# Kernel optimization log

Hardware: AMD Instinct MI355X
Metric: run time of the kernel (lower is better)

Reference implementation:

```python
import jax, jax.numpy as jnp
import numpy as np

NOISE_EPS = 1e-2   # Shazeer noisy-gating stddev floor
LN_EPS = 1e-6
LOSS_COEF = 0.01
K = 2              # num_activated_experts


def _layer_norm(x, w, b):
    mu = jnp.mean(x, axis=-1, keepdims=True)
    var = jnp.var(x, axis=-1, keepdims=True)
    return (x - mu) * jax.lax.rsqrt(var + LN_EPS) * w + b


def _cv_squared(v):
    return jnp.var(v) / (jnp.mean(v) ** 2 + 1e-10)


def _normal_cdf(z):
    return 0.5 * (1.0 + jax.scipy.special.erf(z / jnp.sqrt(jnp.asarray(2.0, z.dtype))))


def setup_inputs() -> dict:
    key = jax.random.key(0)
    ks = jax.random.split(key, 8)
    N, D, H, O, E = 8192, 512, 1024, 512, 8
    x = jax.random.normal(ks[0], (N, D), jnp.float32)
    x_offsets = jnp.sort(jax.random.randint(ks[1], (17,), 0, N)).astype(jnp.int64)
    noise = jax.random.normal(ks[2], (N, E), jnp.float32)
    s = 0.02
    return {
        "x": x,
        "x_offsets": x_offsets,
        "max_seq_len": 2048,
        "noise": noise,
        "norm_w": jnp.ones((D,), jnp.float32),
        "norm_bias": jnp.zeros((D,), jnp.float32),
        "w_gate": jax.random.normal(ks[3], (D, E), jnp.float32) * s,
        "w_noise": jax.random.normal(ks[4], (D, E), jnp.float32) * s,
        "W1": jax.random.normal(ks[5], (E, H, D), jnp.float32) * s,  # [E, model_d, input]
        "b1": jnp.zeros((E, H), jnp.float32),
        "W2": jax.random.normal(ks[6], (E, O, H), jnp.float32) * s,  # [E, output, model_d]
        "b2": jnp.zeros((E, O), jnp.float32),
        "output_weight": jax.random.normal(ks[7], (D, O), jnp.float32) * s,
    }


def reference(x, x_offsets, max_seq_len, noise, norm_w, norm_bias, w_gate, w_noise,
              W1, b1, W2, b2, output_weight):
    N, D = x.shape
    E = w_gate.shape[1]
    k_plus = min(K + 1, E)

    # pre-norm
    x_norm = _layer_norm(x, norm_w, norm_bias)

    # noisy top-k gating (training path)
    clean_logits = x_norm @ w_gate                      # [N, E]
    noise_stddev = jax.nn.softplus(x_norm @ w_noise) + NOISE_EPS
    noisy_logits = clean_logits + noise * noise_stddev

    top_logits, top_indices = jax.lax.top_k(noisy_logits, k_plus)   # [N, k+1]
    top_k_logits = top_logits[:, :K]
    top_k_indices = top_indices[:, :K]
    top_k_gates = jax.nn.softmax(top_k_logits, axis=-1)             # [N, K]

    rows = jnp.arange(N)[:, None]
    gates = jnp.zeros((N, E), top_k_gates.dtype).at[rows, top_k_indices].set(top_k_gates)

    # load = prob each expert is in top-k under the gating noise (Shazeer)
    flat = top_logits.reshape(-1)
    pos_in = jnp.arange(N) * k_plus + K
    thr_in = flat[pos_in][:, None]          # (k+1)-th value: threshold if already in
    thr_out = flat[pos_in - 1][:, None]     # k-th value: threshold if currently out
    is_in = noisy_logits > thr_in
    prob_in = _normal_cdf((clean_logits - thr_in) / noise_stddev)
    prob_out = _normal_cdf((clean_logits - thr_out) / noise_stddev)
    load_probs = jnp.where(is_in, prob_in, prob_out)                # [N, E]

    loss = LOSS_COEF * (_cv_squared(gates.sum(0)) + _cv_squared(load_probs.sum(0)))

    # dispatch stats: tokens per expert
    lengths = jnp.zeros((E,), jnp.float32).at[top_k_indices.reshape(-1)].add(1.0)
    load = lengths / lengths.sum()

    # grouped expert MLP (dense one-hot combine; gates are 0 for unrouted experts)
    h = jnp.einsum('nd,ehd->neh', x_norm, W1) + b1                  # [N, E, H]
    a = jax.nn.silu(h)
    y_e = jnp.einsum('neh,eoh->neo', a, W2) + b2                    # [N, E, O]
    y_moe = jnp.einsum('ne,neo->no', gates, y_e)                    # [N, O]

    # shared expert: addmm(y, shared_x=x, output_weight)
    y = y_moe + x @ output_weight
    return y, loss, load
```

## Files before the change

### kernel.cpp

```cpp
#include <hip/hip_runtime.h>
#include <math.h>

typedef unsigned short u16;
typedef unsigned int u32;

#define N_ROWS 8192
#define DDIM 512
#define HDIM 1024
#define ODIM 512
#define NEXP 8
#define MAXPAIRS (N_ROWS * 2)
#define MAXPOS (MAXPAIRS + NEXP * 128)
#define MAXTILES (MAXPOS / 128)

#define SM_CNT 0
#define SM_CUR 8
#define SM_AOFF 16
#define SM_WORDS 64

using short8 = __attribute__((ext_vector_type(8))) short;
using float4v = __attribute__((ext_vector_type(4))) float;

__device__ __forceinline__ u16 f2bf(float f) {
    union { float f; u32 u; } v; v.f = f;
    u32 u = v.u;
    return (u16)((u + 0x7fffu + ((u >> 16) & 1u)) >> 16);
}

__device__ __forceinline__ void async_copy16(u16* lds, const u16* g) {
    __builtin_amdgcn_global_load_lds(
        (const __attribute__((address_space(1))) void*)g,
        (__attribute__((address_space(3))) void*)lds, 16, 0, 0);
}

#define MEGA_GATE 512
#define MEGA_W1 2048
#define MEGA_OWT 256
#define MEGA_BUCKET 68
#define MEGA_W2 2048
#define MEGA_BLOCKS (MEGA_GATE + MEGA_W1 + MEGA_OWT + MEGA_BUCKET + MEGA_W2)
__global__ __launch_bounds__(256) void mega_kernel(
    const float* __restrict__ x, const float* __restrict__ noise,
    const float* __restrict__ norm_w, const float* __restrict__ norm_b,
    const float* __restrict__ w_gate, const float* __restrict__ w_noise,
    const float* __restrict__ W1, const float* __restrict__ ow,
    const float* __restrict__ W2,
    u16* __restrict__ xnorm_bf, u16* __restrict__ x_bf,
    int* __restrict__ pair_expert, float* __restrict__ pair_gate,
    u16* __restrict__ W1b, u16* __restrict__ owT, u16* __restrict__ W2b,
    int* __restrict__ bucket_rows, int* __restrict__ small, float* __restrict__ zeropage,
    float* __restrict__ partial_g, float* __restrict__ partial_l, int* __restrict__ partial_c)
{
    __shared__ __align__(16) float sh[32 * 33 + 8];
    int b = blockIdx.x, tid = threadIdx.x;

    if (b >= MEGA_GATE) {
        int cb = b - MEGA_GATE;
        if (cb < MEGA_W1) {
            size_t i = (size_t)cb * 512 + tid;
#pragma unroll
            for (int t = 0; t < 2; t++, i += 256) {
                float4 v = ((const float4*)W1)[i];
                ushort4 o;
                o.x = f2bf(v.x); o.y = f2bf(v.y); o.z = f2bf(v.z); o.w = f2bf(v.w);
                ((ushort4*)W1b)[i] = o;
            }
        } else if (cb < MEGA_W1 + MEGA_OWT) {
            float (*tile)[33] = (float(*)[33])sh;
            int t = cb - MEGA_W1;
            int bx = (t & 15) * 32, by = (t >> 4) * 32;
            int tx = tid & 31, ty = tid >> 5;
            for (int r = ty; r < 32; r += 8) tile[r][tx] = ow[(size_t)(by + r) * ODIM + bx + tx];
            __syncthreads();
            for (int r = ty; r < 32; r += 8) owT[(size_t)(bx + r) * DDIM + by + tx] = f2bf(tile[tx][r]);
        } else if (cb < MEGA_W1 + MEGA_OWT + MEGA_BUCKET) {
            int lb = cb - MEGA_W1 - MEGA_OWT;
            int i = lb * 256 + tid;
            if (i < MAXPOS) bucket_rows[i] = -1;
            if (lb == 0) {
                if (tid < SM_WORDS) small[tid] = 0;
                zeropage[tid] = 0.f; zeropage[tid + 256] = 0.f;
            }
        } else {
            int j = cb - MEGA_W1 - MEGA_OWT - MEGA_BUCKET;
            size_t i = (size_t)j * 512 + tid;
#pragma unroll
            for (int t = 0; t < 2; t++, i += 256) {
                float4 v = ((const float4*)W2)[i];
                ushort4 o;
                o.x = f2bf(v.x); o.y = f2bf(v.y); o.z = f2bf(v.z); o.w = f2bf(v.w);
                ((ushort4*)W2b)[i] = o;
            }
        }
        return;
    }

    float* lg = sh;
    float* blk_g = sh + 16 * 17;
    float* blk_l = blk_g + 8;
    int* blk_c = (int*)(blk_l + 8);

    int wave = tid >> 6, lane = tid & 63;
    if (tid < 8) { blk_g[tid] = 0.f; blk_l[tid] = 0.f; blk_c[tid] = 0; }
    float nw[8], nb[8];
#pragma unroll
    for (int j = 0; j < 8; j++) { nw[j] = norm_w[j * 64 + lane]; nb[j] = norm_b[j * 64 + lane]; }

    bool l5 = (lane & 32) != 0, l4 = (lane & 16) != 0;
    bool l3 = (lane & 8) != 0, l2 = (lane & 4) != 0;

    for (int half = 0; half < 2; ++half) {
        float xv[2][8], mu[2], rstd[2];
#pragma unroll
        for (int r = 0; r < 2; ++r) {
            int row = b * 16 + wave * 4 + half * 2 + r;
            const float* xr = x + (size_t)row * DDIM;
            float s = 0.f, s2 = 0.f;
#pragma unroll
            for (int j = 0; j < 8; j++) { float v = xr[j * 64 + lane]; xv[r][j] = v; s += v; s2 += v * v; }
#pragma unroll
            for (int o = 32; o; o >>= 1) { s += __shfl_xor(s, o, 64); s2 += __shfl_xor(s2, o, 64); }
            mu[r] = s * (1.f / DDIM);
            float var = s2 * (1.f / DDIM) - mu[r] * mu[r];
            rstd[r] = rsqrtf(var + 1e-6f);
        }
        float acc[2][16];
#pragma unroll
        for (int r = 0; r < 2; ++r)
#pragma unroll
            for (int e = 0; e < 16; e++) acc[r][e] = 0.f;
#pragma unroll
        for (int j = 0; j < 8; j++) {
            int d = j * 64 + lane;
            float4 wg0 = *(const float4*)&w_gate[d * 8];
            float4 wg1 = *(const float4*)&w_gate[d * 8 + 4];
            float4 wn0 = *(const float4*)&w_noise[d * 8];
            float4 wn1 = *(const float4*)&w_noise[d * 8 + 4];
#pragma unroll
            for (int r = 0; r < 2; ++r) {
                int row = b * 16 + wave * 4 + half * 2 + r;
                float v = (xv[r][j] - mu[r]) * rstd[r] * nw[j] + nb[j];
                xnorm_bf[(size_t)row * DDIM + d] = f2bf(v);
                x_bf[(size_t)row * DDIM + d] = f2bf(xv[r][j]);
                acc[r][0] += v * wg0.x; acc[r][1] += v * wg0.y;
                acc[r][2] += v * wg0.z; acc[r][3] += v * wg0.w;
                acc[r][4] += v * wg1.x; acc[r][5] += v * wg1.y;
                acc[r][6] += v * wg1.z; acc[r][7] += v * wg1.w;
                acc[r][8] += v * wn0.x; acc[r][9] += v * wn0.y;
                acc[r][10] += v * wn0.z; acc[r][11] += v * wn0.w;
                acc[r][12] += v * wn1.x; acc[r][13] += v * wn1.y;
                acc[r][14] += v * wn1.z; acc[r][15] += v * wn1.w;
            }
        }
#pragma unroll
        for (int r = 0; r < 2; ++r) {
            int lrow16 = wave * 4 + half * 2 + r;
            float t8[8];
#pragma unroll
            for (int v = 0; v < 8; v++) {
                float snd = l5 ? acc[r][v] : acc[r][v + 8];
                float kp = l5 ? acc[r][v + 8] : acc[r][v];
                t8[v] = kp + __shfl_xor(snd, 32, 64);
            }
            float t4[4];
#pragma unroll
            for (int v = 0; v < 4; v++) {
                float snd = l4 ? t8[v] : t8[v + 4];
                float kp = l4 ? t8[v + 4] : t8[v];
                t4[v] = kp + __shfl_xor(snd, 16, 64);
            }
            float t2[2];
#pragma unroll
            for (int v = 0; v < 2; v++) {
                float snd = l3 ? t4[v] : t4[v + 2];
                float kp = l3 ? t4[v + 2] : t4[v];
                t2[v] = kp + __shfl_xor(snd, 8, 64);
            }
            float snd = l2 ? t2[0] : t2[1];
            float kp = l2 ? t2[1] : t2[0];
            float t1 = kp + __shfl_xor(snd, 4, 64);
            t1 += __shfl_xor(t1, 2, 64);
            t1 += __shfl_xor(t1, 1, 64);
            if ((lane & 3) == 0) lg[lrow16 * 17 + ((lane >> 2) & 15)] = t1;
        }
    }
    __syncthreads();

    if (tid < 16) {
        int row = b * 16 + tid;
        float cl[8], sd[8], nz[8];
#pragma unroll
        for (int e = 0; e < 8; e++) {
            cl[e] = lg[tid * 17 + e];
            float t = lg[tid * 17 + 8 + e];
            float sp = fmaxf(t, 0.f) + log1pf(expf(-fabsf(t)));
            sd[e] = sp + 0.01f;
            nz[e] = cl[e] + noise[(size_t)row * NEXP + e] * sd[e];
        }
        int idx[3]; float val[3]; u32 msk = 0;
#pragma unroll
        for (int t = 0; t < 3; t++) {
            float best = -INFINITY; int bi = 0;
#pragma unroll
            for (int e = 0; e < 8; e++)
                if (!((msk >> e) & 1) && nz[e] > best) { best = nz[e]; bi = e; }
            idx[t] = bi; val[t] = best; msk |= 1u << bi;
        }
        float e1 = expf(val[1] - val[0]);
        float g0 = 1.f / (1.f + e1), g1 = e1 / (1.f + e1);
        float thr_in = val[2], thr_out = val[1];

        pair_expert[row * 2] = idx[0]; pair_gate[row * 2] = g0;
        pair_expert[row * 2 + 1] = idx[1]; pair_gate[row * 2 + 1] = g1;
        atomicAdd(&blk_g[idx[0]], g0); atomicAdd(&blk_g[idx[1]], g1);
        atomicAdd(&blk_c[idx[0]], 1); atomicAdd(&blk_c[idx[1]], 1);
#pragma unroll
        for (int e = 0; e < 8; e++) {
            float thr = (nz[e] > thr_in) ? thr_in : thr_out;
            float z = (cl[e] - thr) / sd[e];
            float p = 0.5f * (1.f + erff(z * 0.70710678118654752f));
            atomicAdd(&blk_l[e], p);
        }
    }
    __syncthreads();
    if (tid < 8) {
        partial_g[b * 8 + tid] = blk_g[tid];
        partial_l[b * 8 + tid] = blk_l[tid];
        partial_c[b * 8 + tid] = blk_c[tid];
    }
}

__global__ __launch_bounds__(256) void scatter_kernel(
    const int* __restrict__ pair_expert, const float* __restrict__ pair_gate,
    const float* __restrict__ partial_g, const float* __restrict__ partial_l,
    const int* __restrict__ partial_c,
    int* __restrict__ small, int* __restrict__ bucket_rows, float* __restrict__ gate_by_pos,
    int* __restrict__ rowpos,
    float* __restrict__ out_loss, float* __restrict__ out_load)
{
    __shared__ int aoff[NEXP + 1];
    __shared__ int blk_cnt[NEXP];
    __shared__ int blk_base[NEXP];
    __shared__ int ired[256];
    __shared__ float fred[256];
    __shared__ float gsum[NEXP], lsum[NEXP];
    int tid = threadIdx.x;
    int e = tid & 7, g = tid >> 3;

    int s = 0;
    for (int k = g; k < MEGA_GATE; k += 32) s += partial_c[k * 8 + e];
    ired[tid] = s;
    if (tid < NEXP) blk_cnt[tid] = 0;
    __syncthreads();
    if (tid < 64) ired[tid] = ired[tid] + ired[tid + 64] + ired[tid + 128] + ired[tid + 192];
    __syncthreads();
    if (tid < 8) {
        int t = 0;
        for (int q = tid; q < 64; q += 8) t += ired[q];
        ired[tid] = t;
    }
    __syncthreads();
    if (tid == 0) {
        int acc = 0; aoff[0] = 0;
        for (int k = 0; k < NEXP; k++) { acc += (ired[k] + 127) & ~127; aoff[k + 1] = acc; }
    }
    __syncthreads();

    int p = blockIdx.x * 256 + tid;
    int pe = pair_expert[p];
    int local = atomicAdd(&blk_cnt[pe], 1);
    __syncthreads();
    if (tid < NEXP)
        blk_base[tid] = aoff[tid] + atomicAdd(&small[SM_CUR + tid], blk_cnt[tid]);
    if (blockIdx.x == 0 && tid < NEXP + 1) small[SM_AOFF + tid] = aoff[tid];
    __syncthreads();
    int pos = blk_base[pe] + local;
    bucket_rows[pos] = p >> 1;
    gate_by_pos[pos] = pair_gate[p];
    rowpos[p] = pos;

    if (blockIdx.x == 0) {
        float sg = 0.f, sl = 0.f;
        for (int k = g; k < MEGA_GATE; k += 32) { sg += partial_g[k * 8 + e]; sl += partial_l[k * 8 + e]; }
        fred[tid] = sg;
        __syncthreads();
        if (tid < 64) fred[tid] = fred[tid] + fred[tid + 64] + fred[tid + 128] + fred[tid + 192];
        __syncthreads();
        if (tid < 8) { float t = 0.f; for (int q = tid; q < 64; q += 8) t += fred[q]; gsum[tid] = t; }
        __syncthreads();
        fred[tid] = sl;
        __syncthreads();
        if (tid < 64) fred[tid] = fred[tid] + fred[tid + 64] + fred[tid + 128] + fred[tid + 192];
        __syncthreads();
        if (tid < 8) { float t = 0.f; for (int q = tid; q < 64; q += 8) t += fred[q]; lsum[tid] = t; }
        __syncthreads();
        if (tid == 0) {
            float cv[2];
            for (int t = 0; t < 2; t++) {
                const float* v = t ? lsum : gsum;
                float m = 0.f;
                for (int k = 0; k < NEXP; k++) m += v[k];
                m *= (1.f / NEXP);
                float var = 0.f;
                for (int k = 0; k < NEXP; k++) { float d = v[k] - m; var += d * d; }
                var *= (1.f / NEXP);
                cv[t] = var / (m * m + 1e-10f);
            }
            out_loss[0] = 0.01f * (cv[0] + cv[1]);
            int tot = 0;
            for (int k = 0; k < NEXP; k++) tot += ired[k];
            float inv = 1.f / (float)tot;
            for (int k = 0; k < NEXP; k++) out_load[k] = (float)ired[k] * inv;
        }
    }
}

__global__ __launch_bounds__(256) void gemmA_kernel(
    const u16* __restrict__ xnorm, const u16* __restrict__ W1b,
    const u16* __restrict__ xbf, const u16* __restrict__ owT,
    const int* __restrict__ bucket_rows, const int* __restrict__ small,
    const float* __restrict__ b1, const u16* __restrict__ zeropage,
    u16* __restrict__ a_buf, float* __restrict__ y)
{
    constexpr int KD = 512;
    __shared__ __align__(16) u16 As[128 * 64];
    __shared__ __align__(16) u16 Bs[128 * 64];

    int tid = threadIdx.x;
    if (blockIdx.y >= 8) {
        int j = (blockIdx.y - 8) * 136 + blockIdx.x;
        if (j >= 256) return;
        int base = (j >> 2) * 128, bn = (j & 3) * 128;
        int wave = tid >> 6, lane = tid & 63;
        const int lrow = lane >> 2;
        const int kcol = (((lane & 3) ^ ((lane >> 3) & 3)) * 8);
        const int trow = wave * 32 + lrow;
        int wm = (wave & 1) * 64, wn = (wave >> 1) * 64;
        int fr = lane & 15, kq = lane >> 4;
        const int kg = ((kq ^ ((fr >> 1) & 3)) * 8);
        const u16* ga0 = xbf + (size_t)(base + trow) * KD + kcol;
        const u16* ga1 = xbf + (size_t)(base + trow + 16) * KD + kcol;
        const u16* gb0 = owT + (size_t)(bn + trow) * KD + kcol;
        const u16* gb1 = owT + (size_t)(bn + trow + 16) * KD + kcol;
        u16* As2 = (u16*)As; u16* Bs2 = (u16*)Bs;
        const int ofA0 = (wave * 32) * 32, ofA1 = (wave * 32 + 16) * 32;

        float4v acc[4][4];
#pragma unroll
        for (int i = 0; i < 4; i++)
#pragma unroll
            for (int jj = 0; jj < 4; jj++) acc[i][jj] = (float4v){0.f, 0.f, 0.f, 0.f};

        async_copy16(As2 + ofA0, ga0); async_copy16(As2 + ofA1, ga1);
        async_copy16(Bs2 + ofA0, gb0); async_copy16(Bs2 + ofA1, gb1);
        __syncthreads();
        int cur = 0;
        for (int t = 0; t < 16; ++t) {
            int nxt = cur ^ 1;
            if (t + 1 < 16) {
                int k1 = (t + 1) << 5;
                async_copy16(As2 + nxt * 4096 + ofA0, ga0 + k1);
                async_copy16(As2 + nxt * 4096 + ofA1, ga1 + k1);
                async_copy16(Bs2 + nxt * 4096 + ofA0, gb0 + k1);
                async_copy16(Bs2 + nxt * 4096 + ofA1, gb1 + k1);
            }
            short8 af[4], bf[4];
#pragma unroll
            for (int mt = 0; mt < 4; mt++) af[mt] = *(const short8*)&As2[cur * 4096 + (wm + mt * 16 + fr) * 32 + kg];
#pragma unroll
            for (int nt = 0; nt < 4; nt++) bf[nt] = *(const short8*)&Bs2[cur * 4096 + (wn + nt * 16 + fr) * 32 + kg];
#pragma unroll
            for (int mt = 0; mt < 4; mt++)
#pragma unroll
                for (int nt = 0; nt < 4; nt++)
                    acc[mt][nt] = __builtin_amdgcn_mfma_f32_16x16x32_bf16(af[mt], bf[nt], acc[mt][nt], 0, 0, 0);
            __syncthreads();
            cur = nxt;
        }
        int rbase = (lane >> 4) * 4, c16 = lane & 15;
#pragma unroll
        for (int mt = 0; mt < 4; mt++) {
            int gm = base + wm + mt * 16 + rbase;
#pragma unroll
            for (int nt = 0; nt < 4; nt++) {
                int gn = bn + wn + nt * 16 + c16;
#pragma unroll
                for (int r = 0; r < 4; r++)
                    y[(size_t)(gm + r) * ODIM + gn] = acc[mt][nt][r];
            }
        }
        return;
    }

    int base = blockIdx.x * 128;
    if (base >= small[SM_AOFF + 8]) return;
    int e = 0;
    while (e < 7 && base >= small[SM_AOFF + e + 1]) ++e;
    int bn = blockIdx.y * 128;
    const u16* Bsel = W1b + (size_t)e * HDIM * KD;

    int wave = tid >> 6, lane = tid & 63;
    int lr = lane >> 3;
    int lc = ((lane & 7) ^ lr) * 8;

    const u16* ga[4]; const u16* gb[4];
    u16* la[4]; u16* lb[4];
#pragma unroll
    for (int c = 0; c < 4; c++) {
        int tr = wave * 32 + c * 8;
        int r0 = bucket_rows[base + tr + lr];
        ga[c] = ((r0 < 0) ? zeropage : xnorm + (size_t)r0 * KD) + lc;
        gb[c] = Bsel + (size_t)(bn + tr + lr) * KD + lc;
        la[c] = &As[tr * 64];
        lb[c] = &Bs[tr * 64];
    }

    int wm = (wave & 1) * 64, wn = (wave >> 1) * 64;
    int fr = lane & 15, kq = lane >> 4, f7 = fr & 7;

    float4v acc[4][4];
#pragma unroll
    for (int i = 0; i < 4; i++)
#pragma unroll
        for (int j = 0; j < 4; j++) acc[i][j] = (float4v){0.f, 0.f, 0.f, 0.f};

    for (int k0 = 0; k0 < KD; k0 += 64) {
        __syncthreads();
#pragma unroll
        for (int c = 0; c < 4; c++) async_copy16(la[c], ga[c] + k0);
#pragma unroll
        for (int c = 0; c < 4; c++) async_copy16(lb[c], gb[c] + k0);
        __syncthreads();
        short8 af[4][2], bf[4][2];
#pragma unroll
        for (int mt = 0; mt < 4; mt++)
#pragma unroll
            for (int kh = 0; kh < 2; kh++)
                af[mt][kh] = *(const short8*)&As[(wm + mt * 16 + fr) * 64 + (((kq + 4 * kh) ^ f7) * 8)];
#pragma unroll
        for (int nt = 0; nt < 4; nt++)
#pragma unroll
            for (int kh = 0; kh < 2; kh++)
                bf[nt][kh] = *(const short8*)&Bs[(wn + nt * 16 + fr) * 64 + (((kq + 4 * kh) ^ f7) * 8)];
#pragma unroll
        for (int mt = 0; mt < 4; mt++)
#pragma unroll
            for (int nt = 0; nt < 4; nt++) {
                acc[mt][nt] = __builtin_amdgcn_mfma_f32_16x16x32_bf16(af[mt][0], bf[nt][0], acc[mt][nt], 0, 0, 0);
                acc[mt][nt] = __builtin_amdgcn_mfma_f32_16x16x32_bf16(af[mt][1], bf[nt][1], acc[mt][nt], 0, 0, 0);
            }
    }

    int rbase = (lane >> 4) * 4, c16 = lane & 15;
#pragma unroll
    for (int nt = 0; nt < 4; nt++) {
        int gn = bn + wn + nt * 16 + c16;
        float bv = b1[e * HDIM + gn];
#pragma unroll
        for (int mt = 0; mt < 4; mt++) {
            int gm = base + wm + mt * 16 + rbase;
#pragma unroll
            for (int r = 0; r < 4; r++) {
                float h = acc[mt][nt][r] + bv;
                float a = h * __builtin_amdgcn_rcpf(1.f + __expf(-h));
                a_buf[(size_t)(gm + r) * HDIM + gn] = f2bf(a);
            }
        }
    }
}

__global__ __launch_bounds__(512) void gemmB_kernel(
    const u16* __restrict__ a_buf, const u16* __restrict__ W2b,
    const int* __restrict__ bucket_rows, const int* __restrict__ small,
    const float* __restrict__ b2, const float* __restrict__ gate_by_pos,
    float* __restrict__ ye)
{
    constexpr int KD = 1024;
    __shared__ __align__(16) u16 As[2][128 * 32];
    __shared__ __align__(16) u16 Bs[2][256 * 32];

    int tid = threadIdx.x;
    int wave = tid >> 6, lane = tid & 63;
    const int lrow = lane >> 2;
    const int kcol = (((lane & 3) ^ ((lane >> 3) & 3)) * 8);
    int wm = (wave >> 2) * 64, wn = (wave & 3) * 64;
    int fr = lane & 15, kq = lane >> 4;
    const int kg = ((kq ^ ((fr >> 1) & 3)) * 8);

    int base = blockIdx.x * 128;
    if (base >= small[SM_AOFF + 8]) return;
    int e = 0;
    while (e < 7 && base >= small[SM_AOFF + e + 1]) ++e;
    int bn = blockIdx.y * 256;

    const u16* ga0 = a_buf + (size_t)(base + wave * 16 + lrow) * KD + kcol;
    const u16* Bsel = W2b + (size_t)e * ODIM * KD;
    const u16* gb0 = Bsel + (size_t)(bn + wave * 32 + lrow) * KD + kcol;
    const u16* gb1 = Bsel + (size_t)(bn + wave * 32 + 16 + lrow) * KD + kcol;
    const int ofA = (wave * 16) * 32;
    const int ofB0 = (wave * 32) * 32;
    const int ofB1 = (wave * 32 + 16) * 32;

    float4v acc[4][4];
#pragma unroll
    for (int i = 0; i < 4; i++)
#pragma unroll
        for (int j = 0; j < 4; j++) acc[i][j] = (float4v){0.f, 0.f, 0.f, 0.f};

    constexpr int nk = KD >> 5;
    async_copy16(&As[0][ofA], ga0);
    async_copy16(&Bs[0][ofB0], gb0);
    async_copy16(&Bs[0][ofB1], gb1);
    __syncthreads();

    int cur = 0;
    for (int t = 0; t < nk; ++t) {
        int nxt = cur ^ 1;
        if (t + 1 < nk) {
            int k1 = (t + 1) << 5;
            async_copy16(&As[nxt][ofA], ga0 + k1);
            async_copy16(&Bs[nxt][ofB0], gb0 + k1);
            async_copy16(&Bs[nxt][ofB1], gb1 + k1);
        }
        short8 af[4], bf[4];
#pragma unroll
        for (int mt = 0; mt < 4; mt++) af[mt] = *(const short8*)&As[cur][(wm + mt * 16 + fr) * 32 + kg];
#pragma unroll
        for (int nt = 0; nt < 4; nt++) bf[nt] = *(const short8*)&Bs[cur][(wn + nt * 16 + fr) * 32 + kg];
#pragma unroll
        for (int mt = 0; mt < 4; mt++)
#pragma unroll
            for (int nt = 0; nt < 4; nt++)
                acc[mt][nt] = __builtin_amdgcn_mfma_f32_16x16x32_bf16(af[mt], bf[nt], acc[mt][nt], 0, 0, 0);
        __syncthreads();
        cur = nxt;
    }

    int rbase = (lane >> 4) * 4, c16 = lane & 15;
#pragma unroll
    for (int mt = 0; mt < 4; mt++) {
        int pos0 = base + wm + mt * 16 + rbase;
        int rows[4]; float gs[4];
#pragma unroll
        for (int r = 0; r < 4; r++) { rows[r] = bucket_rows[pos0 + r]; gs[r] = gate_by_pos[pos0 + r]; }
#pragma unroll
        for (int nt = 0; nt < 4; nt++) {
            int gn = bn + wn + nt * 16 + c16;
            float b2v = b2[e * ODIM + gn];
#pragma unroll
            for (int r = 0; r < 4; r++) {
                if (rows[r] >= 0)
                    ye[(size_t)(pos0 + r) * ODIM + gn] = gs[r] * (acc[mt][nt][r] + b2v);
            }
        }
    }
}

__global__ __launch_bounds__(256) void combine_kernel(
    const float* __restrict__ ye, const int* __restrict__ rowpos,
    float* __restrict__ y)
{
    int tid = threadIdx.x;
    int row = blockIdx.x * 16 + (tid >> 4);
    int c0 = (tid & 15) * 32;
    int p0 = rowpos[row * 2];
    int p1 = rowpos[row * 2 + 1];
    const float4* e0 = (const float4*)(ye + (size_t)p0 * ODIM + c0);
    const float4* e1 = (const float4*)(ye + (size_t)p1 * ODIM + c0);
    float4* yp = (float4*)(y + (size_t)row * ODIM + c0);
#pragma unroll
    for (int i = 0; i < 8; i++) {
        float4 a = yp[i], b = e0[i], c = e1[i];
        a.x += b.x + c.x; a.y += b.y + c.y; a.z += b.z + c.z; a.w += b.w + c.w;
        yp[i] = a;
    }
}

extern "C" void kernel_launch(void* const* d_in, const int* in_sizes, int n_in,
                              void* d_out, int out_size, void* d_ws, size_t ws_size,
                              hipStream_t stream)
{
    (void)in_sizes; (void)n_in; (void)out_size; (void)ws_size;
    const float* x = (const float*)d_in[0];
    const float* noise = (const float*)d_in[3];
    const float* norm_w = (const float*)d_in[4];
    const float* norm_b = (const float*)d_in[5];
    const float* w_gate = (const float*)d_in[6];
    const float* w_noise = (const float*)d_in[7];
    const float* W1 = (const float*)d_in[8];
    const float* b1 = (const float*)d_in[9];
    const float* W2 = (const float*)d_in[10];
    const float* b2 = (const float*)d_in[11];
    const float* ow = (const float*)d_in[12];

    float* y = (float*)d_out;
    float* out_loss = y + (size_t)N_ROWS * ODIM;
    float* out_load = out_loss + 1;

    char* ws = (char*)d_ws;
    size_t off = 0;
    auto alloc = [&](size_t b) { size_t p = off; off = (off + b + 255) & ~(size_t)255; return p; };
    u16* xnorm_bf = (u16*)(ws + alloc((size_t)N_ROWS * DDIM * 2));
    u16* x_bf     = (u16*)(ws + alloc((size_t)N_ROWS * DDIM * 2));
    u16* W1b      = (u16*)(ws + alloc((size_t)NEXP * HDIM * DDIM * 2));
    u16* W2b      = (u16*)(ws + alloc((size_t)NEXP * ODIM * HDIM * 2));
    u16* owT      = (u16*)(ws + alloc((size_t)DDIM * ODIM * 2));
    u16* a_buf    = (u16*)(ws + alloc((size_t)MAXPOS * HDIM * 2));
    float* ye     = (float*)(ws + alloc((size_t)MAXPOS * ODIM * 4));
    int* pair_expert = (int*)(ws + alloc((size_t)MAXPAIRS * 4));
    float* pair_gate = (float*)(ws + alloc((size_t)MAXPAIRS * 4));
    float* gate_by_pos = (float*)(ws + alloc((size_t)MAXPOS * 4));
    int* bucket_rows = (int*)(ws + alloc((size_t)MAXPOS * 4));
    int* rowpos      = (int*)(ws + alloc((size_t)MAXPAIRS * 4));
    int* small       = (int*)(ws + alloc(SM_WORDS * 4));
    float* zeropage  = (float*)(ws + alloc(2048));
    float* partial_g = (float*)(ws + alloc((size_t)MEGA_GATE * NEXP * 4));
    float* partial_l = (float*)(ws + alloc((size_t)MEGA_GATE * NEXP * 4));
    int* partial_c   = (int*)(ws + alloc((size_t)MEGA_GATE * NEXP * 4));

    mega_kernel<<<MEGA_BLOCKS, 256, 0, stream>>>(
        x, noise, norm_w, norm_b, w_gate, w_noise, W1, ow, W2,
        xnorm_bf, x_bf, pair_expert, pair_gate, W1b, owT, W2b,
        bucket_rows, small, zeropage, partial_g, partial_l, partial_c);
    scatter_kernel<<<MAXPAIRS / 256, 256, 0, stream>>>(pair_expert, pair_gate,
                                                       partial_g, partial_l, partial_c,
                                                       small, bucket_rows, gate_by_pos, rowpos,
                                                       out_loss, out_load);
    gemmA_kernel<<<dim3(MAXTILES, 8 + 2), 256, 0, stream>>>(xnorm_bf, W1b,
                                                            x_bf, owT, bucket_rows, small, b1,
                                                            (const u16*)zeropage, a_buf, y);
    gemmB_kernel<<<dim3(MAXTILES, 2), 512, 0, stream>>>(a_buf, W2b, bucket_rows,
                                                        small, b2, gate_by_pos, ye);
    combine_kernel<<<N_ROWS / 16, 256, 0, stream>>>(ye, rowpos, y);
}
```

Baseline: 237.9 us.

## Enlarge gemmA tiles to 128x256 with 512 threads and double-buffered K=32 pipeline

The first expert GEMM and the shared-expert GEMM now use a 128x256 output tile computed by 8 waves, mirroring gemmB's layout. The expert path also moves from a single-buffered K=64 loop with two barriers per step to a double-buffered K=32 async-copy pipeline. The grid changes from 10 to 5 y-slices. This aims to halve A-tile reloads, overlap global loads with MFMA work and cut per-block overhead, at the cost of fewer blocks in flight and more shared memory per block.

```diff
diff --git a/kernel.cpp b/kernel.cpp
--- a/kernel.cpp
+++ b/kernel.cpp
@@ -315,7 +315,7 @@
     }
 }
 
-__global__ __launch_bounds__(256) void gemmA_kernel(
+__global__ __launch_bounds__(512) void gemmA_kernel(
     const u16* __restrict__ xnorm, const u16* __restrict__ W1b,
     const u16* __restrict__ xbf, const u16* __restrict__ owT,
     const int* __restrict__ bucket_rows, const int* __restrict__ small,
@@ -323,61 +323,96 @@
     u16* __restrict__ a_buf, float* __restrict__ y)
 {
     constexpr int KD = 512;
-    __shared__ __align__(16) u16 As[128 * 64];
-    __shared__ __align__(16) u16 Bs[128 * 64];
+    __shared__ __align__(16) u16 As[2][128 * 32];
+    __shared__ __align__(16) u16 Bs[2][256 * 32];
 
     int tid = threadIdx.x;
-    if (blockIdx.y >= 8) {
-        int j = (blockIdx.y - 8) * 136 + blockIdx.x;
-        if (j >= 256) return;
-        int base = (j >> 2) * 128, bn = (j & 3) * 128;
-        int wave = tid >> 6, lane = tid & 63;
-        const int lrow = lane >> 2;
-        const int kcol = (((lane & 3) ^ ((lane >> 3) & 3)) * 8);
-        const int trow = wave * 32 + lrow;
-        int wm = (wave & 1) * 64, wn = (wave >> 1) * 64;
-        int fr = lane & 15, kq = lane >> 4;
-        const int kg = ((kq ^ ((fr >> 1) & 3)) * 8);
-        const u16* ga0 = xbf + (size_t)(base + trow) * KD + kcol;
-        const u16* ga1 = xbf + (size_t)(base + trow + 16) * KD + kcol;
-        const u16* gb0 = owT + (size_t)(bn + trow) * KD + kcol;
-        const u16* gb1 = owT + (size_t)(bn + trow + 16) * KD + kcol;
-        u16* As2 = (u16*)As; u16* Bs2 = (u16*)Bs;
-        const int ofA0 = (wave * 32) * 32, ofA1 = (wave * 32 + 16) * 32;
-
-        float4v acc[4][4];
-#pragma unroll
-        for (int i = 0; i < 4; i++)
-#pragma unroll
-            for (int jj = 0; jj < 4; jj++) acc[i][jj] = (float4v){0.f, 0.f, 0.f, 0.f};
-
-        async_copy16(As2 + ofA0, ga0); async_copy16(As2 + ofA1, ga1);
-        async_copy16(Bs2 + ofA0, gb0); async_copy16(Bs2 + ofA1, gb1);
-        __syncthreads();
-        int cur = 0;
-        for (int t = 0; t < 16; ++t) {
-            int nxt = cur ^ 1;
-            if (t + 1 < 16) {
-                int k1 = (t + 1) << 5;
-                async_copy16(As2 + nxt * 4096 + ofA0, ga0 + k1);
-                async_copy16(As2 + nxt * 4096 + ofA1, ga1 + k1);
-                async_copy16(Bs2 + nxt * 4096 + ofA0, gb0 + k1);
-                async_copy16(Bs2 + nxt * 4096 + ofA1, gb1 + k1);
-            }
-            short8 af[4], bf[4];
-#pragma unroll
-            for (int mt = 0; mt < 4; mt++) af[mt] = *(const short8*)&As2[cur * 4096 + (wm + mt * 16 + fr) * 32 + kg];
-#pragma unroll
-            for (int nt = 0; nt < 4; nt++) bf[nt] = *(const short8*)&Bs2[cur * 4096 + (wn + nt * 16 + fr) * 32 + kg];
-#pragma unroll
-            for (int mt = 0; mt < 4; mt++)
-#pragma unroll
-                for (int nt = 0; nt < 4; nt++)
-                    acc[mt][nt] = __builtin_amdgcn_mfma_f32_16x16x32_bf16(af[mt], bf[nt], acc[mt][nt], 0, 0, 0);
-            __syncthreads();
-            cur = nxt;
-        }
-        int rbase = (lane >> 4) * 4, c16 = lane & 15;
+    int wave = tid >> 6, lane = tid & 63;
+    const int lrow = lane >> 2;
+    const int kcol = (((lane & 3) ^ ((lane >> 3) & 3)) * 8);
+    int wm = (wave >> 2) * 64, wn = (wave & 3) * 64;
+    int fr = lane & 15, kq = lane >> 4;
+    const int kg = ((kq ^ ((fr >> 1) & 3)) * 8);
+
+    bool m0 = blockIdx.y < 4;
+    int base, bn, e = 0;
+    const u16 *ga0, *gb0, *gb1;
+    if (m0) {
+        base = blockIdx.x * 128;
+        if (base >= small[SM_AOFF + 8]) return;
+        while (e < 7 && base >= small[SM_AOFF + e + 1]) ++e;
+        bn = blockIdx.y * 256;
+        int r0 = bucket_rows[base + wave * 16 + lrow];
+        ga0 = ((r0 < 0) ? zeropage : xnorm + (size_t)r0 * KD) + kcol;
+        const u16* Bsel = W1b + (size_t)e * HDIM * KD;
+        gb0 = Bsel + (size_t)(bn + wave * 32 + lrow) * KD + kcol;
+        gb1 = Bsel + (size_t)(bn + wave * 32 + 16 + lrow) * KD + kcol;
+    } else {
+        int j = blockIdx.x;
+        if (j >= 128) return;
+        base = (j >> 1) * 128;
+        bn = (j & 1) * 256;
+        ga0 = xbf + (size_t)(base + wave * 16 + lrow) * KD + kcol;
+        gb0 = owT + (size_t)(bn + wave * 32 + lrow) * KD + kcol;
+        gb1 = owT + (size_t)(bn + wave * 32 + 16 + lrow) * KD + kcol;
+    }
+    const int ofA = (wave * 16) * 32;
+    const int ofB0 = (wave * 32) * 32;
+    const int ofB1 = (wave * 32 + 16) * 32;
+
+    float4v acc[4][4];
+#pragma unroll
+    for (int i = 0; i < 4; i++)
+#pragma unroll
+        for (int j = 0; j < 4; j++) acc[i][j] = (float4v){0.f, 0.f, 0.f, 0.f};
+
+    constexpr int nk = KD >> 5;
+    async_copy16(&As[0][ofA], ga0);
+    async_copy16(&Bs[0][ofB0], gb0);
+    async_copy16(&Bs[0][ofB1], gb1);
+    __syncthreads();
+
+    int cur = 0;
+    for (int t = 0; t < nk; ++t) {
+        int nxt = cur ^ 1;
+        if (t + 1 < nk) {
+            int k1 = (t + 1) << 5;
+            async_copy16(&As[nxt][ofA], ga0 + k1);
+            async_copy16(&Bs[nxt][ofB0], gb0 + k1);
+            async_copy16(&Bs[nxt][ofB1], gb1 + k1);
+        }
+        short8 af[4], bf[4];
+#pragma unroll
+        for (int mt = 0; mt < 4; mt++) af[mt] = *(const short8*)&As[cur][(wm + mt * 16 + fr) * 32 + kg];
+#pragma unroll
+        for (int nt = 0; nt < 4; nt++) bf[nt] = *(const short8*)&Bs[cur][(wn + nt * 16 + fr) * 32 + kg];
+#pragma unroll
+        for (int mt = 0; mt < 4; mt++)
+#pragma unroll
+            for (int nt = 0; nt < 4; nt++)
+                acc[mt][nt] = __builtin_amdgcn_mfma_f32_16x16x32_bf16(af[mt], bf[nt], acc[mt][nt], 0, 0, 0);
+        __syncthreads();
+        cur = nxt;
+    }
+
+    int rbase = (lane >> 4) * 4, c16 = lane & 15;
+    if (m0) {
+#pragma unroll
+        for (int nt = 0; nt < 4; nt++) {
+            int gn = bn + wn + nt * 16 + c16;
+            float bv = b1[e * HDIM + gn];
+#pragma unroll
+            for (int mt = 0; mt < 4; mt++) {
+                int gm = base + wm + mt * 16 + rbase;
+#pragma unroll
+                for (int r = 0; r < 4; r++) {
+                    float h = acc[mt][nt][r] + bv;
+                    float a = h * __builtin_amdgcn_rcpf(1.f + __expf(-h));
+                    a_buf[(size_t)(gm + r) * HDIM + gn] = f2bf(a);
+                }
+            }
+        }
+    } else {
 #pragma unroll
         for (int mt = 0; mt < 4; mt++) {
             int gm = base + wm + mt * 16 + rbase;
@@ -387,83 +422,6 @@
 #pragma unroll
                 for (int r = 0; r < 4; r++)
                     y[(size_t)(gm + r) * ODIM + gn] = acc[mt][nt][r];
-            }
-        }
-        return;
-    }
-
-    int base = blockIdx.x * 128;
-    if (base >= small[SM_AOFF + 8]) return;
-    int e = 0;
-    while (e < 7 && base >= small[SM_AOFF + e + 1]) ++e;
-    int bn = blockIdx.y * 128;
-    const u16* Bsel = W1b + (size_t)e * HDIM * KD;
-
-    int wave = tid >> 6, lane = tid & 63;
-    int lr = lane >> 3;
-    int lc = ((lane & 7) ^ lr) * 8;
-
-    const u16* ga[4]; const u16* gb[4];
-    u16* la[4]; u16* lb[4];
-#pragma unroll
-    for (int c = 0; c < 4; c++) {
-        int tr = wave * 32 + c * 8;
-        int r0 = bucket_rows[base + tr + lr];
-        ga[c] = ((r0 < 0) ? zeropage : xnorm + (size_t)r0 * KD) + lc;
-        gb[c] = Bsel + (size_t)(bn + tr + lr) * KD + lc;
-        la[c] = &As[tr * 64];
-        lb[c] = &Bs[tr * 64];
-    }
-
-    int wm = (wave & 1) * 64, wn = (wave >> 1) * 64;
-    int fr = lane & 15, kq = lane >> 4, f7 = fr & 7;
-
-    float4v acc[4][4];
-#pragma unroll
-    for (int i = 0; i < 4; i++)
-#pragma unroll
-        for (int j = 0; j < 4; j++) acc[i][j] = (float4v){0.f, 0.f, 0.f, 0.f};
-
-    for (int k0 = 0; k0 < KD; k0 += 64) {
-        __syncthreads();
-#pragma unroll
-        for (int c = 0; c < 4; c++) async_copy16(la[c], ga[c] + k0);
-#pragma unroll
-        for (int c = 0; c < 4; c++) async_copy16(lb[c], gb[c] + k0);
-        __syncthreads();
-        short8 af[4][2], bf[4][2];
-#pragma unroll
-        for (int mt = 0; mt < 4; mt++)
-#pragma unroll
-            for (int kh = 0; kh < 2; kh++)
-                af[mt][kh] = *(const short8*)&As[(wm + mt * 16 + fr) * 64 + (((kq + 4 * kh) ^ f7) * 8)];
-#pragma unroll
-        for (int nt = 0; nt < 4; nt++)
-#pragma unroll
-            for (int kh = 0; kh < 2; kh++)
-                bf[nt][kh] = *(const short8*)&Bs[(wn + nt * 16 + fr) * 64 + (((kq + 4 * kh) ^ f7) * 8)];
-#pragma unroll
-        for (int mt = 0; mt < 4; mt++)
-#pragma unroll
-            for (int nt = 0; nt < 4; nt++) {
-                acc[mt][nt] = __builtin_amdgcn_mfma_f32_16x16x32_bf16(af[mt][0], bf[nt][0], acc[mt][nt], 0, 0, 0);
-                acc[mt][nt] = __builtin_amdgcn_mfma_f32_16x16x32_bf16(af[mt][1], bf[nt][1], acc[mt][nt], 0, 0, 0);
-            }
-    }
-
-    int rbase = (lane >> 4) * 4, c16 = lane & 15;
-#pragma unroll
-    for (int nt = 0; nt < 4; nt++) {
-        int gn = bn + wn + nt * 16 + c16;
-        float bv = b1[e * HDIM + gn];
-#pragma unroll
-        for (int mt = 0; mt < 4; mt++) {
-            int gm = base + wm + mt * 16 + rbase;
-#pragma unroll
-            for (int r = 0; r < 4; r++) {
-                float h = acc[mt][nt][r] + bv;
-                float a = h * __builtin_amdgcn_rcpf(1.f + __expf(-h));
-                a_buf[(size_t)(gm + r) * HDIM + gn] = f2bf(a);
             }
         }
     }
@@ -626,9 +584,9 @@
                                                        partial_g, partial_l, partial_c,
                                                        small, bucket_rows, gate_by_pos, rowpos,
                                                        out_loss, out_load);
-    gemmA_kernel<<<dim3(MAXTILES, 8 + 2), 256, 0, stream>>>(xnorm_bf, W1b,
-                                                            x_bf, owT, bucket_rows, small, b1,
-                                                            (const u16*)zeropage, a_buf, y);
+    gemmA_kernel<<<dim3(MAXTILES, 5), 512, 0, stream>>>(xnorm_bf, W1b,
+                                                        x_bf, owT, bucket_rows, small, b1,
+                                                        (const u16*)zeropage, a_buf, y);
     gemmB_kernel<<<dim3(MAXTILES, 2), 512, 0, stream>>>(a_buf, W2b, bucket_rows,
                                                         small, b2, gate_by_pos, ye);
     combine_kernel<<<N_ROWS / 16, 256, 0, stream>>>(ye, rowpos, y);
```

After: 234.5 us. About the same (-1.4%).
